# Kernel tuning notes

Hardware: AMD Instinct MI355X
Metric: run time of the kernel (lower is better)

The kernel has to match this reference:

```python
import jax, jax.numpy as jnp
import numpy as np

N = 2048          # num agents / graph nodes
D = 128           # n_actor == n_map
ALPHA = 0.2       # GAT leakyrelu alpha
NEG = -1e9
X_IDX = [4, 9, 14, 19]   # actors_inter_cat time indices per LSTM step
E_IDX = [0, 4, 9, 14]    # graph_adjs time indices per LSTM step


def setup_inputs() -> dict:
    key = jax.random.key(0)
    ks = jax.random.split(key, 10)
    xavier = lambda k, shape: jax.random.uniform(
        k, shape, jnp.float32, -1.0, 1.0) * 1.414 * np.sqrt(6.0 / (shape[-2] + shape[-1]))
    actors_inter_cat = jax.random.normal(ks[0], (N, 20, D), jnp.float32)
    graph_adjs = jax.random.randint(ks[1], (N, 20, N), 0, 2, jnp.int32)
    # 4 GAT_SRF gates (forget, input, input_cell, output), stacked on leading axis
    Wg = xavier(ks[2], (4, 2 * D, D))          # gate projection W: in=2*D, out=D
    ag = xavier(ks[3], (4, 2 * D))             # attention vector a (2*out_features,)
    W = xavier(ks[4], (D, D))                  # GAT cell output projection
    b = xavier(ks[5], (1, D))
    h0 = xavier(ks[6], (1, D))
    conv_w = jax.random.normal(ks[7], (3, D, D, 2), jnp.float32) * (1.0 / np.sqrt(2 * D))
    conv_b = jax.random.normal(ks[8], (3, D), jnp.float32) * 0.01
    return {"actors_inter_cat": actors_inter_cat, "graph_adjs": graph_adjs,
            "Wg": Wg, "ag": ag, "W": W, "b": b, "h0": h0,
            "conv_w": conv_w, "conv_b": conv_b}


def _gat_gates(gin, mask, Wg, ag):
    # gin: (N, 2D); mask: (N, N) bool. Computes all 4 GAT_SRF gates at once.
    Wh = jnp.einsum('nf,gfo->gno', gin, Wg)                 # (4, N, D)
    s_src = jnp.einsum('gno,go->gn', Wh, ag[:, :D])         # a^T [Wh_i ..]
    s_dst = jnp.einsum('gno,go->gn', Wh, ag[:, D:])
    e = jax.nn.leaky_relu(s_src[:, :, None] + s_dst[:, None, :], ALPHA)  # (4,N,N)
    e = jnp.where(mask[None], e, NEG)
    attn = jax.nn.softmax(e, axis=-1)
    return jax.nn.elu(jnp.einsum('gnm,gmo->gno', attn, Wh))  # concat=True -> ELU


def reference(actors_inter_cat, graph_adjs, Wg, ag, W, b, h0, conv_w, conv_b):
    n = actors_inter_cat.shape[0]
    cell = actors_inter_cat[:, 0, :]
    hidden = jnp.broadcast_to(h0, (n, D))
    outs = []
    for t in range(4):  # fixed 4-step recurrence
        X = actors_inter_cat[:, X_IDX[t], :]
        mask = graph_adjs[:, E_IDX[t], :] > 0
        gin = jnp.concatenate([X, hidden], axis=1)          # (N, 2D)
        g = _gat_gates(gin, mask, Wg, ag)                   # (4, N, D)
        forget = jax.nn.sigmoid(g[0])
        inp_gate = jax.nn.sigmoid(g[1])
        inp_cell = jnp.tanh(g[2])
        out_gate = jax.nn.sigmoid(g[3])
        cell = cell * forget + inp_gate * inp_cell
        hidden = jnp.tanh(cell) * out_gate
        outs.append(jax.nn.sigmoid(hidden @ W + b))
    y = jnp.stack(outs, axis=2)                             # (N, D, 4)
    for l in range(3):  # kernel-2 Conv1d stack: length 4 -> 3 -> 2 -> 1
        y = (jnp.einsum('nct,oc->not', y[:, :, :-1], conv_w[l, :, :, 0])
             + jnp.einsum('nct,oc->not', y[:, :, 1:], conv_w[l, :, :, 1])
             + conv_b[l][None, :, None])
    return y[:, :, 0]                                       # squeeze -> (N, D)
```

## Files before the change

kernel.cpp:

```cpp
#include <hip/hip_runtime.h>

typedef __attribute__((ext_vector_type(8))) short short8;
typedef __attribute__((ext_vector_type(4))) float floatx4;

#define MFMA16(a,b,c) __builtin_amdgcn_mfma_f32_16x16x32_bf16(a,b,c,0,0,0)

__device__ __forceinline__ unsigned short f2bf(float f){
  unsigned u = __float_as_uint(f);
  u += 0x7fffu + ((u >> 16) & 1u);
  return (unsigned short)(u >> 16);
}
__device__ __forceinline__ float sigm(float x){ return 1.f/(1.f+__expf(-x)); }


__global__ __launch_bounds__(256) void prep_kernel(const float* __restrict__ actors,
    const float* __restrict__ Wg, const float* __restrict__ cw, const int* __restrict__ adj,
    float* __restrict__ cell, unsigned short* __restrict__ WgA, float* __restrict__ cwT,
    unsigned long long* __restrict__ bm){
  int bid = blockIdx.x;
  if (bid < 1024){
    int idx = bid*256 + threadIdx.x;
    int n = idx >> 7, c = idx & 127;
    cell[idx] = actors[(size_t)n*2560 + c];
  } else if (bid < 1536){
    int e = (bid-1024)*256 + threadIdx.x;
    int g = e >> 15, o = (e >> 8) & 127, k = e & 255;
    unsigned short v = f2bf(Wg[(size_t)g*32768 + k*128 + o]);
    int off = ((o>>4)*8 + (k>>5))*512 + (((k>>3)&3)*16 + (o&15))*8 + (k&7);
    WgA[(size_t)g*32768 + off] = v;
  } else if (bid < 1728){
    int e = (bid-1536)*256 + threadIdx.x;
    int l = e >> 14, rr = e & 16383, k = rr >> 7, o = rr & 127;
    cwT[(size_t)l*32768 + k*256 + o]       = cw[(size_t)l*32768 + o*256 + k*2];
    cwT[(size_t)l*32768 + k*256 + 128 + o] = cw[(size_t)l*32768 + o*256 + k*2 + 1];
  } else {
    const int E[4] = {0,4,9,14};
    int mb = bid - 1728;
    int t = mb & 3, nblk = mb >> 2;
    int wv = threadIdx.x >> 6, lane = threadIdx.x & 63;
    int n = nblk*4 + wv;
    const int* row = adj + (size_t)n*40960 + (size_t)E[t]*2048;
    unsigned long long* outp = bm + ((size_t)t*2048 + n)*32;
    for (int it=0; it<32; ++it){
      unsigned long long bal = __ballot(row[it*64 + lane] > 0);
      if (lane == 0) outp[it] = bal;
    }
  }
}

__global__ __launch_bounds__(512,2) void gatewh_kernel(const float* __restrict__ actors,
    const float* __restrict__ gbuf, float* __restrict__ cell, const float* __restrict__ h0,
    const float* __restrict__ W, const float* __restrict__ bvec,
    const unsigned short* __restrict__ WgA, const float* __restrict__ ag,
    float* __restrict__ y, unsigned short* __restrict__ WhB,
    float* __restrict__ spart, int xoff, int t){
  __shared__ float hl[16][132];
  __shared__ __align__(16) unsigned short ginb[16*264];
  __shared__ float sredS[4][4][16], sredD[4][4][16];
  int bx = blockIdx.x;
  int tile = bx >> 1, ohalf = bx & 1;
  int n0 = tile*16, tid = threadIdx.x;
  int row = tid>>5, q = tid&31;
  {
    int o0 = q*4;
    if (t == 0){
      *(float4*)&hl[row][o0] = *(const float4*)(h0 + o0);
    } else {
      size_t idx = (size_t)(n0+row)*128 + o0;
      float4 ga = *(const float4*)(gbuf+idx);
      float4 gb = *(const float4*)(gbuf+262144+idx);
      float4 gc = *(const float4*)(gbuf+524288+idx);
      float4 gd = *(const float4*)(gbuf+786432+idx);
      float4 cv = *(const float4*)(cell+idx);
      float fg[4]={ga.x,ga.y,ga.z,ga.w}, ig[4]={gb.x,gb.y,gb.z,gb.w};
      float ic[4]={gc.x,gc.y,gc.z,gc.w}, og[4]={gd.x,gd.y,gd.z,gd.w};
      float cc[4]={cv.x,cv.y,cv.z,cv.w};
      float clv[4];
      #pragma unroll
      for (int j=0;j<4;++j){
        clv[j] = cc[j]*sigm(fg[j]) + sigm(ig[j])*tanhf(ic[j]);
        hl[row][o0+j] = tanhf(clv[j])*sigm(og[j]);
      }
      if (ohalf == 0)
        *(float4*)(cell+idx) = (float4){clv[0],clv[1],clv[2],clv[3]};
    }
  }
  __syncthreads();
  if (t >= 1){
    int oc = ohalf*64 + q*2;
    float2 bb2 = *(const float2*)(bvec+oc);
    float a0 = bb2.x, a1 = bb2.y;
    const float* hr = hl[row];
    for (int k=0;k<128;++k){
      float hv = hr[k];
      float2 wv = *(const float2*)(W + (size_t)k*128 + oc);
      a0 += hv*wv.x; a1 += hv*wv.y;
    }
    float* yp = y + (size_t)(t-1)*262144 + (size_t)(n0+row)*128 + oc;
    yp[0] = sigm(a0); yp[1] = sigm(a1);
  }
  if (q < 16){
    const float* ap = actors + (size_t)(n0+row)*2560 + xoff + q*8;
    float4 a = *(const float4*)ap, bb = *(const float4*)(ap+4);
    unsigned short tmp[8] = {f2bf(a.x),f2bf(a.y),f2bf(a.z),f2bf(a.w),
                             f2bf(bb.x),f2bf(bb.y),f2bf(bb.z),f2bf(bb.w)};
    *(uint4*)&ginb[row*264 + q*8] = *(const uint4*)tmp;
  } else {
    int c0 = (q-16)*8;
    unsigned short tmp[8];
    #pragma unroll
    for (int j=0;j<8;++j) tmp[j] = f2bf(hl[row][c0+j]);
    *(uint4*)&ginb[row*264 + 128 + c0] = *(const uint4*)tmp;
  }
  __syncthreads();
  int w = tid>>6, lane = tid&63, quad = lane>>4, l16 = lane&15;
  int m32 = tile>>1, min32 = (tile&1)*16 + l16;
  int qp = min32>>3, jp = min32&7;
  #pragma unroll
  for (int ci=0; ci<2; ++ci){
    int cidx = w*2 + ci;
    int g = cidx>>2, o16q = cidx&3, o16 = ohalf*4 + o16q;
    floatx4 acc = {0.f,0.f,0.f,0.f};
    const unsigned short* wa = WgA + (size_t)g*32768;
    #pragma unroll
    for (int kh=0; kh<8; ++kh){
      short8 bfr = *(const short8*)&ginb[l16*264 + kh*32 + quad*8];
      short8 a0 = *(const short8*)(wa + (size_t)((o16*8 + kh)*64 + lane)*8);
      acc = MFMA16(a0, bfr, acc);
    }
    float ps = 0.f, pd = 0.f;
    unsigned short* wb = WhB + (size_t)(g*8 + o16)*32768 + m32*512 + qp*128 + jp;
    const float* agp = ag + g*256;
    #pragma unroll
    for (int r=0;r<4;++r){
      int o = o16*16 + quad*4 + r;
      float v = acc[r];
      ps += v*agp[o]; pd += v*agp[128+o];
      wb[(quad*4+r)*8] = f2bf(v);
    }
    ps += __shfl_down(ps,32); ps += __shfl_down(ps,16);
    pd += __shfl_down(pd,32); pd += __shfl_down(pd,16);
    if (lane < 16){ sredS[g][o16q][l16] = ps; sredD[g][o16q][l16] = pd; }
  }
  __syncthreads();
  if (tid < 128){
    int g = tid>>5, which = (tid>>4)&1, n = tid&15;
    float s;
    if (which) s = sredD[g][0][n]+sredD[g][1][n]+sredD[g][2][n]+sredD[g][3][n];
    else       s = sredS[g][0][n]+sredS[g][1][n]+sredS[g][2][n]+sredS[g][3][n];
    spart[(size_t)((ohalf*2 + which)*4 + g)*2048 + n0 + n] = s;
  }
}

__global__ __launch_bounds__(512,2) void attn_kernel(const unsigned char* __restrict__ bmb,
    const unsigned short* __restrict__ WhB, const float* __restrict__ spart,
    float* __restrict__ gout, int t){
  __shared__ float obuf[4][32][132];
  __shared__ float zpart[8][32];
  int bid = blockIdx.x;
  int g = bid & 3, n0 = (bid >> 2)*32;
  int tid = threadIdx.x;
  int w = tid>>6, lane = tid&63, quad = lane>>4, l16 = lane&15;
  const float* sS0 = spart + (size_t)(0 + g)*2048;
  const float* sD0 = spart + (size_t)(4 + g)*2048;
  const float* sS1 = spart + (size_t)(8 + g)*2048;
  const float* sD1 = spart + (size_t)(12 + g)*2048;
  float srcv0 = sS0[n0 + l16]      + sS1[n0 + l16];
  float srcv1 = sS0[n0 + 16 + l16] + sS1[n0 + 16 + l16];
  const unsigned char* mr0 = bmb + ((size_t)t*2048 + n0 + l16)*256 + w*32;
  const unsigned char* mr1 = mr0 + 16*256;
  uint4 q0 = *(const uint4*)mr0, q1 = *(const uint4*)(mr0+16);
  uint4 r0 = *(const uint4*)mr1, r1 = *(const uint4*)(mr1+16);
  unsigned mwd0[8] = {q0.x,q0.y,q0.z,q0.w, q1.x,q1.y,q1.z,q1.w};
  unsigned mwd1[8] = {r0.x,r0.y,r0.z,r0.w, r1.x,r1.y,r1.z,r1.w};
  const unsigned short* wb = WhB + (size_t)g*262144;
  float z0 = 0.f, z1 = 0.f;
  floatx4 acc0[8], acc1[8];
  #pragma unroll
  for (int j=0;j<8;++j){ acc0[j] = (floatx4){0.f,0.f,0.f,0.f}; acc1[j] = acc0[j]; }
  short8 Bf[2][8];
  float4 sp[2][4];
  {
    const unsigned short* bp = wb + (size_t)(w*8 + 0)*512 + lane*8;
    #pragma unroll
    for (int o16=0;o16<8;++o16) Bf[0][o16] = *(const short8*)(bp + (size_t)o16*32768);
    int mk = w*256 + quad*8;
    sp[0][0] = *(const float4*)(sD0 + mk); sp[0][1] = *(const float4*)(sD0 + mk + 4);
    sp[0][2] = *(const float4*)(sD1 + mk); sp[0][3] = *(const float4*)(sD1 + mk + 4);
  }
  #pragma unroll
  for (int c=0; c<8; ++c){
    const int cur = c & 1, nxt = cur ^ 1;
    if (c < 7){
      const unsigned short* bp = wb + (size_t)(w*8 + c + 1)*512 + lane*8;
      #pragma unroll
      for (int o16=0;o16<8;++o16) Bf[nxt][o16] = *(const short8*)(bp + (size_t)o16*32768);
      int mk2 = w*256 + (c+1)*32 + quad*8;
      sp[nxt][0] = *(const float4*)(sD0 + mk2); sp[nxt][1] = *(const float4*)(sD0 + mk2 + 4);
      sp[nxt][2] = *(const float4*)(sD1 + mk2); sp[nxt][3] = *(const float4*)(sD1 + mk2 + 4);
    }
    unsigned mb0 = (mwd0[c] >> (quad*8)) & 0xffu;
    unsigned mb1 = (mwd1[c] >> (quad*8)) & 0xffu;
    float4 sa0 = sp[cur][0], sb0 = sp[cur][1], sa1 = sp[cur][2], sb1 = sp[cur][3];
    float sv[8] = {sa0.x+sa1.x, sa0.y+sa1.y, sa0.z+sa1.z, sa0.w+sa1.w,
                   sb0.x+sb1.x, sb0.y+sb1.y, sb0.z+sb1.z, sb0.w+sb1.w};
    short8 A0, A1;
    #pragma unroll
    for (int j=0;j<8;++j){
      float s0 = srcv0 + sv[j];
      s0 = fmaxf(s0, 0.2f*s0);
      float p0 = ((mb0 >> j) & 1u) ? __expf(s0) : 0.f;
      z0 += p0;
      A0[j] = (short)f2bf(p0);
      float s1 = srcv1 + sv[j];
      s1 = fmaxf(s1, 0.2f*s1);
      float p1 = ((mb1 >> j) & 1u) ? __expf(s1) : 0.f;
      z1 += p1;
      A1[j] = (short)f2bf(p1);
    }
    #pragma unroll
    for (int o16=0; o16<8; ++o16){
      acc0[o16] = MFMA16(A0, Bf[cur][o16], acc0[o16]);
      acc1[o16] = MFMA16(A1, Bf[cur][o16], acc1[o16]);
    }
  }
  z0 += __shfl_down(z0,32); z0 += __shfl_down(z0,16);
  z1 += __shfl_down(z1,32); z1 += __shfl_down(z1,16);
  if (lane < 16){ zpart[w][l16] = z0; zpart[w][16+l16] = z1; }
  if (w < 4){
    #pragma unroll
    for (int o16=0;o16<8;++o16)
      #pragma unroll
      for (int r=0;r<4;++r){
        obuf[w][quad*4+r][o16*16+l16]      = acc0[o16][r];
        obuf[w][16+quad*4+r][o16*16+l16]   = acc1[o16][r];
      }
  }
  __syncthreads();
  if (w >= 4){
    #pragma unroll
    for (int o16=0;o16<8;++o16)
      #pragma unroll
      for (int r=0;r<4;++r){
        obuf[w-4][quad*4+r][o16*16+l16]    += acc0[o16][r];
        obuf[w-4][16+quad*4+r][o16*16+l16] += acc1[o16][r];
      }
  }
  __syncthreads();
  {
    int row = tid>>4, c0 = (tid&15)*8;
    float z = zpart[0][row]+zpart[1][row]+zpart[2][row]+zpart[3][row]
            + zpart[4][row]+zpart[5][row]+zpart[6][row]+zpart[7][row];
    float inv = 1.f / z;
    float* go = gout + (size_t)g*262144 + (size_t)(n0+row)*128 + c0;
    #pragma unroll
    for (int j=0;j<8;++j){
      float v = (obuf[0][row][c0+j] + obuf[1][row][c0+j]
               + obuf[2][row][c0+j] + obuf[3][row][c0+j]) * inv;
      go[j] = v > 0.f ? v : __expf(v) - 1.f;
    }
  }
}

__global__ __launch_bounds__(256) void convgate_kernel(const float* __restrict__ gbuf,
    const float* __restrict__ cell, const float* __restrict__ W, const float* __restrict__ bvec,
    const float* __restrict__ y, const float* __restrict__ cwT, const float* __restrict__ cb,
    float* __restrict__ out){
  __shared__ float hl[4][128];
  __shared__ float ylds[4][128][4];
  int tid = threadIdx.x;
  int r = tid >> 6, oc = (tid & 63)*2;
  int n = blockIdx.x*4 + r;
  size_t idx = (size_t)n*128 + oc;
  {
    float2 g0 = *(const float2*)(gbuf+idx),        g1 = *(const float2*)(gbuf+262144+idx);
    float2 g2 = *(const float2*)(gbuf+524288+idx), g3 = *(const float2*)(gbuf+786432+idx);
    float2 cv = *(const float2*)(cell+idx);
    float fg[2]={g0.x,g0.y}, ig[2]={g1.x,g1.y}, ic[2]={g2.x,g2.y}, og[2]={g3.x,g3.y};
    float cc[2]={cv.x,cv.y};
    #pragma unroll
    for (int j=0;j<2;++j){
      float cl = cc[j]*sigm(fg[j]) + sigm(ig[j])*tanhf(ic[j]);
      hl[r][oc+j] = tanhf(cl)*sigm(og[j]);
    }
  }
  {
    float2 y0 = *(const float2*)(y+idx), y1 = *(const float2*)(y+262144+idx),
           y2 = *(const float2*)(y+524288+idx);
    float a0[2]={y0.x,y0.y}, a1[2]={y1.x,y1.y}, a2[2]={y2.x,y2.y};
    #pragma unroll
    for (int j=0;j<2;++j){
      ylds[r][oc+j][0]=a0[j]; ylds[r][oc+j][1]=a1[j]; ylds[r][oc+j][2]=a2[j];
    }
  }
  __syncthreads();
  {
    float2 bb = *(const float2*)(bvec+oc);
    float acc[2] = {bb.x, bb.y};
    const float* hr = hl[r];
    for (int k=0;k<128;++k){
      float hv = hr[k];
      float2 wv = *(const float2*)(W + (size_t)k*128 + oc);
      acc[0]+=hv*wv.x; acc[1]+=hv*wv.y;
    }
    #pragma unroll
    for (int j=0;j<2;++j) ylds[r][oc+j][3] = sigm(acc[j]);
  }
  __syncthreads();
  {
    float a0[2]={0,0}, a1[2]={0,0}, a2[2]={0,0};
    for (int k=0;k<128;++k){
      float2 w0 = *(const float2*)(cwT + k*256 + oc);
      float2 w1 = *(const float2*)(cwT + k*256 + 128 + oc);
      float4 yv = *(const float4*)&ylds[r][k][0];
      float wa[2]={w0.x,w0.y}, wb2[2]={w1.x,w1.y};
      #pragma unroll
      for (int j=0;j<2;++j){
        a0[j] += yv.x*wa[j] + yv.y*wb2[j];
        a1[j] += yv.y*wa[j] + yv.z*wb2[j];
        a2[j] += yv.z*wa[j] + yv.w*wb2[j];
      }
    }
    float2 bb = *(const float2*)(cb+oc);
    float bbv[2]={bb.x,bb.y};
    __syncthreads();
    #pragma unroll
    for (int j=0;j<2;++j){
      ylds[r][oc+j][0]=a0[j]+bbv[j]; ylds[r][oc+j][1]=a1[j]+bbv[j]; ylds[r][oc+j][2]=a2[j]+bbv[j];
    }
    __syncthreads();
  }
  {
    float a0[2]={0,0}, a1[2]={0,0};
    for (int k=0;k<128;++k){
      float2 w0 = *(const float2*)(cwT + 32768 + k*256 + oc);
      float2 w1 = *(const float2*)(cwT + 32768 + k*256 + 128 + oc);
      float4 yv = *(const float4*)&ylds[r][k][0];
      float wa[2]={w0.x,w0.y}, wb2[2]={w1.x,w1.y};
      #pragma unroll
      for (int j=0;j<2;++j){
        a0[j] += yv.x*wa[j] + yv.y*wb2[j];
        a1[j] += yv.y*wa[j] + yv.z*wb2[j];
      }
    }
    float2 bb = *(const float2*)(cb+128+oc);
    float bbv[2]={bb.x,bb.y};
    __syncthreads();
    #pragma unroll
    for (int j=0;j<2;++j){
      ylds[r][oc+j][0]=a0[j]+bbv[j]; ylds[r][oc+j][1]=a1[j]+bbv[j];
    }
    __syncthreads();
  }
  {
    float a0[2]={0,0};
    for (int k=0;k<128;++k){
      float2 w0 = *(const float2*)(cwT + 65536 + k*256 + oc);
      float2 w1 = *(const float2*)(cwT + 65536 + k*256 + 128 + oc);
      float4 yv = *(const float4*)&ylds[r][k][0];
      a0[0] += yv.x*w0.x + yv.y*w1.x;
      a0[1] += yv.x*w0.y + yv.y*w1.y;
    }
    float2 bb = *(const float2*)(cb+256+oc);
    float2 res = {a0[0]+bb.x, a0[1]+bb.y};
    *(float2*)(out+idx) = res;
  }
}

extern "C" void kernel_launch(void* const* d_in, const int* in_sizes, int n_in,
                              void* d_out, int out_size, void* d_ws, size_t ws_size,
                              hipStream_t stream) {
  const float* actors = (const float*)d_in[0];
  const int*   adj    = (const int*)d_in[1];
  const float* Wg     = (const float*)d_in[2];
  const float* ag     = (const float*)d_in[3];
  const float* W      = (const float*)d_in[4];
  const float* b      = (const float*)d_in[5];
  const float* h0     = (const float*)d_in[6];
  const float* cw     = (const float*)d_in[7];
  const float* cb     = (const float*)d_in[8];
  float* out = (float*)d_out;

  char* ws = (char*)d_ws;
  unsigned long long* bm = (unsigned long long*)ws;
  float* cell          = (float*)(ws + (size_t)(2u<<20));
  unsigned short* WgA  = (unsigned short*)(ws + (size_t)(3u<<20));
  float* cwT           = (float*)(ws + (size_t)3407872);
  float* spart         = (float*)(ws + (size_t)3932160);
  unsigned short* WhB  = (unsigned short*)(ws + (size_t)(4u<<20));
  float* gbuf          = (float*)(ws + (size_t)(7u<<20));
  float* yplanes       = (float*)(ws + (size_t)(11u<<20));

  const int XI[4] = {4, 9, 14, 19};

  prep_kernel<<<3776, 256, 0, stream>>>(actors, Wg, cw, adj, cell, WgA, cwT, bm);
  for (int t=0; t<4; ++t){
    gatewh_kernel<<<256, 512, 0, stream>>>(actors, gbuf, cell, h0, W, b, WgA, ag,
                                           yplanes, WhB, spart, XI[t]*128, t);
    attn_kernel<<<256, 512, 0, stream>>>((const unsigned char*)bm, WhB,
                                         spart, gbuf, t);
  }
  convgate_kernel<<<512, 256, 0, stream>>>(gbuf, cell, W, b, yplanes, cwT, cb, out);
}
```

Baseline: 590.5 us.

## Stage Wh tiles via direct global-to-LDS async loads in attention kernel

The attention kernel no longer double-buffers Wh B-fragments in registers. It issues global_load_lds copies into a 128KB LDS double buffer, uses explicit vmcnt waits and reads the fragments back from LDS before each MFMA. The summed destination scores are precomputed once into shared memory instead of being reloaded from global and added per chunk, and obuf now reuses the staging buffer after a barrier. This is meant to cut register pressure and VGPR load latency, but 136KB+ of LDS per block likely breaks the 2-blocks-per-CU occupancy and adds LDS read traffic. An unroll pragma is also added to the output projection loop.

```diff
diff --git a/kernel.cpp b/kernel.cpp
--- a/kernel.cpp
+++ b/kernel.cpp
@@ -91,6 +91,7 @@
     float2 bb2 = *(const float2*)(bvec+oc);
     float a0 = bb2.x, a1 = bb2.y;
     const float* hr = hl[row];
+    #pragma unroll 8
     for (int k=0;k<128;++k){
       float hv = hr[k];
       float2 wv = *(const float2*)(W + (size_t)k*128 + oc);
@@ -155,7 +156,8 @@
 __global__ __launch_bounds__(512,2) void attn_kernel(const unsigned char* __restrict__ bmb,
     const unsigned short* __restrict__ WhB, const float* __restrict__ spart,
     float* __restrict__ gout, int t){
-  __shared__ float obuf[4][32][132];
+  __shared__ __align__(16) unsigned char smem[131072];
+  __shared__ float ssum[2048];
   __shared__ float zpart[8][32];
   int bid = blockIdx.x;
   int g = bid & 3, n0 = (bid >> 2)*32;
@@ -165,6 +167,21 @@
   const float* sD0 = spart + (size_t)(4 + g)*2048;
   const float* sS1 = spart + (size_t)(8 + g)*2048;
   const float* sD1 = spart + (size_t)(12 + g)*2048;
+  const unsigned short* wb = WhB + (size_t)g*262144;
+  const unsigned short* wbw = wb + (size_t)(w*8)*512;
+
+  {
+    unsigned char* lp0 = smem + (size_t)w*8192;
+    #pragma unroll
+    for (int o16=0;o16<8;++o16)
+      __builtin_amdgcn_global_load_lds((const void*)(wbw + (size_t)o16*32768 + lane*8),
+                                       (void*)(lp0 + o16*1024), 16, 0, 0);
+  }
+  {
+    float4 d0 = *(const float4*)(sD0 + tid*4);
+    float4 d1 = *(const float4*)(sD1 + tid*4);
+    *(float4*)&ssum[tid*4] = (float4){d0.x+d1.x, d0.y+d1.y, d0.z+d1.z, d0.w+d1.w};
+  }
   float srcv0 = sS0[n0 + l16]      + sS1[n0 + l16];
   float srcv1 = sS0[n0 + 16 + l16] + sS1[n0 + 16 + l16];
   const unsigned char* mr0 = bmb + ((size_t)t*2048 + n0 + l16)*256 + w*32;
@@ -173,37 +190,32 @@
   uint4 r0 = *(const uint4*)mr1, r1 = *(const uint4*)(mr1+16);
   unsigned mwd0[8] = {q0.x,q0.y,q0.z,q0.w, q1.x,q1.y,q1.z,q1.w};
   unsigned mwd1[8] = {r0.x,r0.y,r0.z,r0.w, r1.x,r1.y,r1.z,r1.w};
-  const unsigned short* wb = WhB + (size_t)g*262144;
   float z0 = 0.f, z1 = 0.f;
   floatx4 acc0[8], acc1[8];
   #pragma unroll
   for (int j=0;j<8;++j){ acc0[j] = (floatx4){0.f,0.f,0.f,0.f}; acc1[j] = acc0[j]; }
-  short8 Bf[2][8];
-  float4 sp[2][4];
-  {
-    const unsigned short* bp = wb + (size_t)(w*8 + 0)*512 + lane*8;
-    #pragma unroll
-    for (int o16=0;o16<8;++o16) Bf[0][o16] = *(const short8*)(bp + (size_t)o16*32768);
-    int mk = w*256 + quad*8;
-    sp[0][0] = *(const float4*)(sD0 + mk); sp[0][1] = *(const float4*)(sD0 + mk + 4);
-    sp[0][2] = *(const float4*)(sD1 + mk); sp[0][3] = *(const float4*)(sD1 + mk + 4);
-  }
+
   #pragma unroll
   for (int c=0; c<8; ++c){
-    const int cur = c & 1, nxt = cur ^ 1;
+    const int cur = c & 1;
     if (c < 7){
-      const unsigned short* bp = wb + (size_t)(w*8 + c + 1)*512 + lane*8;
-      #pragma unroll
-      for (int o16=0;o16<8;++o16) Bf[nxt][o16] = *(const short8*)(bp + (size_t)o16*32768);
-      int mk2 = w*256 + (c+1)*32 + quad*8;
-      sp[nxt][0] = *(const float4*)(sD0 + mk2); sp[nxt][1] = *(const float4*)(sD0 + mk2 + 4);
-      sp[nxt][2] = *(const float4*)(sD1 + mk2); sp[nxt][3] = *(const float4*)(sD1 + mk2 + 4);
-    }
+      unsigned char* lp = smem + (size_t)(((c+1)&1)*8 + w)*8192;
+      const unsigned short* gsrc = wbw + (size_t)(c+1)*512 + lane*8;
+      #pragma unroll
+      for (int o16=0;o16<8;++o16)
+        __builtin_amdgcn_global_load_lds((const void*)(gsrc + (size_t)o16*32768),
+                                         (void*)(lp + o16*1024), 16, 0, 0);
+      asm volatile("s_waitcnt vmcnt(8)" ::: "memory");
+    } else {
+      asm volatile("s_waitcnt vmcnt(0)" ::: "memory");
+    }
+    __builtin_amdgcn_sched_barrier(0);
+    int mk = w*256 + c*32 + quad*8;
+    float4 sa = *(const float4*)&ssum[mk];
+    float4 sb = *(const float4*)&ssum[mk+4];
+    float sv[8] = {sa.x,sa.y,sa.z,sa.w, sb.x,sb.y,sb.z,sb.w};
     unsigned mb0 = (mwd0[c] >> (quad*8)) & 0xffu;
     unsigned mb1 = (mwd1[c] >> (quad*8)) & 0xffu;
-    float4 sa0 = sp[cur][0], sb0 = sp[cur][1], sa1 = sp[cur][2], sb1 = sp[cur][3];
-    float sv[8] = {sa0.x+sa1.x, sa0.y+sa1.y, sa0.z+sa1.z, sa0.w+sa1.w,
-                   sb0.x+sb1.x, sb0.y+sb1.y, sb0.z+sb1.z, sb0.w+sb1.w};
     short8 A0, A1;
     #pragma unroll
     for (int j=0;j<8;++j){
@@ -218,15 +230,19 @@
       z1 += p1;
       A1[j] = (short)f2bf(p1);
     }
+    const unsigned char* sb_base = smem + (size_t)(cur*8 + w)*8192 + lane*16;
     #pragma unroll
     for (int o16=0; o16<8; ++o16){
-      acc0[o16] = MFMA16(A0, Bf[cur][o16], acc0[o16]);
-      acc1[o16] = MFMA16(A1, Bf[cur][o16], acc1[o16]);
+      short8 bfr = *(const short8*)(sb_base + o16*1024);
+      acc0[o16] = MFMA16(A0, bfr, acc0[o16]);
+      acc1[o16] = MFMA16(A1, bfr, acc1[o16]);
     }
   }
   z0 += __shfl_down(z0,32); z0 += __shfl_down(z0,16);
   z1 += __shfl_down(z1,32); z1 += __shfl_down(z1,16);
   if (lane < 16){ zpart[w][l16] = z0; zpart[w][16+l16] = z1; }
+  __syncthreads();
+  float (*obuf)[32][132] = (float (*)[32][132])smem;
   if (w < 4){
     #pragma unroll
     for (int o16=0;o16<8;++o16)
```

Result: no change. 584.4 us (-1.0%).
